# Performance work log

Measured on AMD Instinct MI355X. Metric: run time of the kernel, lower is better.

The kernel has to match this reference:

```python
import jax, jax.numpy as jnp
import numpy as np

NB_CAT = 8192       # nb_category per column
RANK = 16           # low-rank factor dimension
N_COLS = 4          # number of categorical columns (len(embedding_sizes))
N_PAIRS = 1048576   # number of (x, y) index pairs
FRAC_DIAG = 0.9     # fraction_diagonal init


def setup_inputs() -> dict:
    key = jax.random.key(0)
    k1, k2, k3, k4 = jax.random.split(key, 4)
    x = jax.random.randint(k1, (N_PAIRS, N_COLS), 0, NB_CAT, dtype=jnp.int32)
    y = jax.random.randint(k2, (N_PAIRS, N_COLS), 0, NB_CAT, dtype=jnp.int32)
    # params initialized as in the torch module, plus small noise so values are non-degenerate
    std = (FRAC_DIAG * jnp.ones((N_COLS, NB_CAT), dtype=jnp.float32)
           + 0.01 * jax.random.normal(k3, (N_COLS, NB_CAT), dtype=jnp.float32))
    covar_factor = ((1.0 - FRAC_DIAG) / np.float32(np.sqrt(RANK))
                    * jnp.ones((N_COLS, NB_CAT, RANK), dtype=jnp.float32)
                    + 0.01 * jax.random.normal(k4, (N_COLS, NB_CAT, RANK), dtype=jnp.float32))
    return {"x": x, "y": y, "covar_factor": covar_factor, "std": std}


def reference(x, y, covar_factor, std):
    # Build full covariance per column: F @ F.T + diag(std^2)   -> [C, N, N]
    cov = jnp.einsum('cnr,cmr->cnm', covar_factor, covar_factor)
    diag_idx = jnp.arange(cov.shape[1])
    cov = cov.at[:, diag_idx, diag_idx].add(std * std)
    # Gather requested (x, y) entries per column, then reduce (should_reduce=True)
    cols = jnp.arange(cov.shape[0])  # [C]
    vals = cov[cols[None, :], x, y]  # [B, C]
    return vals.sum(axis=-1)         # [B]
```

## Files before the change

### kernel.cpp

```cpp
#include <hip/hip_runtime.h>

#define NB_CAT  8192
#define RANK    16
#define N_COLS  4
#define N_PAIRS 1048576

#define SLICE_ROWS  NB_CAT
#define SLICE_BYTES (SLICE_ROWS * 16)
#define TBL_BYTES   ((size_t)N_COLS * SLICE_BYTES)
#define LDS_BYTES   SLICE_BYTES

typedef float float2v __attribute__((ext_vector_type(2)));

#if defined(__HIP_DEVICE_COMPILE__) && defined(__has_builtin)
#if __has_builtin(__builtin_amdgcn_cvt_pk_f32_fp8) && __has_builtin(__builtin_amdgcn_cvt_pk_fp8_f32)
#define DEV_FP8_HW 1
#endif
#endif

template <int C> __device__ __forceinline__ int comp(const int4& v) {
    if (C == 0) return v.x;
    if (C == 1) return v.y;
    if (C == 2) return v.z;
    return v.w;
}

__device__ __forceinline__ float sw_dec_fp8(unsigned int b) {
    const unsigned int s = b >> 7, e = (b >> 3) & 0xF, m = b & 7;
    float v;
    if (e == 0) v = (float)m * 0.001953125f;
    else        v = ldexpf((float)(8 + m), (int)e - 10);
    return s ? -v : v;
}
__device__ __forceinline__ unsigned int sw_enc_fp8(float f) {
    const unsigned int s = (__float_as_uint(f) >> 31) << 7;
    float a = fabsf(f);
    if (a > 448.f) a = 448.f;
    float q;
    if (a >= 0.015625f) {
        int ex; const float m = frexpf(a, &ex);
        q = ldexpf(rintf(ldexpf(m, 4)), ex - 4);
    } else {
        q = rintf(a * 512.f) * 0.001953125f;
    }
    if (q == 0.f) return s;
    int ex; const float m = frexpf(q, &ex);
    if (ex - 1 < -6) {
        const unsigned int mm = (unsigned int)rintf(q * 512.f);
        return s | (mm & 7);
    }
    const unsigned int e = (unsigned int)(ex - 1 + 7);
    const unsigned int mm = (unsigned int)rintf(ldexpf(m, 4)) & 7;
    return s | (e << 3) | mm;
}

template <bool HI>
__device__ __forceinline__ float2v dec2(unsigned int u) {
#ifdef DEV_FP8_HW
    return __builtin_amdgcn_cvt_pk_f32_fp8((int)u, HI);
#else
    const unsigned int w = HI ? (u >> 16) : u;
    float2v r;
    r.x = sw_dec_fp8(w & 0xFF);
    r.y = sw_dec_fp8((w >> 8) & 0xFF);
    return r;
#endif
}

__device__ __forceinline__ float dot16_fp8(uint4 A, uint4 B, float acc) {
#define TERM(u, v, SEL)                                                        \
    {                                                                          \
        const float2v a = dec2<SEL>((u));                                      \
        const float2v b = dec2<SEL>((v));                                      \
        acc = fmaf(a.x, b.x, acc);                                             \
        acc = fmaf(a.y, b.y, acc);                                             \
    }
    TERM(A.x, B.x, false) TERM(A.x, B.x, true)
    TERM(A.y, B.y, false) TERM(A.y, B.y, true)
    TERM(A.z, B.z, false) TERM(A.z, B.z, true)
    TERM(A.w, B.w, false) TERM(A.w, B.w, true)
#undef TERM
    return acc;
}

__global__ __launch_bounds__(256) void pack_fp8_kernel(
    const float4* __restrict__ src, uint4* __restrict__ dst)
{
    const int r = blockIdx.x * 256 + threadIdx.x;
    const float4 f0 = src[r * 4 + 0];
    const float4 f1 = src[r * 4 + 1];
    const float4 f2 = src[r * 4 + 2];
    const float4 f3 = src[r * 4 + 3];
    uint4 u;
#ifdef DEV_FP8_HW
    int w;
    w = 0;
    w = __builtin_amdgcn_cvt_pk_fp8_f32(f0.x, f0.y, w, false);
    w = __builtin_amdgcn_cvt_pk_fp8_f32(f0.z, f0.w, w, true);
    u.x = (unsigned int)w;
    w = 0;
    w = __builtin_amdgcn_cvt_pk_fp8_f32(f1.x, f1.y, w, false);
    w = __builtin_amdgcn_cvt_pk_fp8_f32(f1.z, f1.w, w, true);
    u.y = (unsigned int)w;
    w = 0;
    w = __builtin_amdgcn_cvt_pk_fp8_f32(f2.x, f2.y, w, false);
    w = __builtin_amdgcn_cvt_pk_fp8_f32(f2.z, f2.w, w, true);
    u.z = (unsigned int)w;
    w = 0;
    w = __builtin_amdgcn_cvt_pk_fp8_f32(f3.x, f3.y, w, false);
    w = __builtin_amdgcn_cvt_pk_fp8_f32(f3.z, f3.w, w, true);
    u.w = (unsigned int)w;
#else
    u.x = sw_enc_fp8(f0.x) | (sw_enc_fp8(f0.y) << 8) | (sw_enc_fp8(f0.z) << 16) | (sw_enc_fp8(f0.w) << 24);
    u.y = sw_enc_fp8(f1.x) | (sw_enc_fp8(f1.y) << 8) | (sw_enc_fp8(f1.z) << 16) | (sw_enc_fp8(f1.w) << 24);
    u.z = sw_enc_fp8(f2.x) | (sw_enc_fp8(f2.y) << 8) | (sw_enc_fp8(f2.z) << 16) | (sw_enc_fp8(f2.w) << 24);
    u.w = sw_enc_fp8(f3.x) | (sw_enc_fp8(f3.y) << 8) | (sw_enc_fp8(f3.z) << 16) | (sw_enc_fp8(f3.w) << 24);
#endif
    dst[r] = u;
}

__global__ __launch_bounds__(1024, 1) void IndexKernel_32238024524411_kernel(
    const int4*  __restrict__ x4,
    const int4*  __restrict__ y4,
    const uint4* __restrict__ tbl,
    const float* __restrict__ stdv,
    float*       __restrict__ out)
{
    extern __shared__ uint4 sh[];

    const int tid  = threadIdx.x;
    const int base = blockIdx.x * 4096 + tid;

    int4 xv[4], yv[4];
#pragma unroll
    for (int j = 0; j < 4; ++j) {
        xv[j] = x4[base + j * 1024];
        yv[j] = y4[base + j * 1024];
    }

    float acc[4] = {0.f, 0.f, 0.f, 0.f};

#pragma unroll
    for (int j = 0; j < 4; ++j) {
        const int4 a = xv[j], b = yv[j];
        if (a.x == b.x) { const float s = stdv[0 * NB_CAT + a.x]; acc[j] = fmaf(s, s, acc[j]); }
        if (a.y == b.y) { const float s = stdv[1 * NB_CAT + a.y]; acc[j] = fmaf(s, s, acc[j]); }
        if (a.z == b.z) { const float s = stdv[2 * NB_CAT + a.z]; acc[j] = fmaf(s, s, acc[j]); }
        if (a.w == b.w) { const float s = stdv[3 * NB_CAT + a.w]; acc[j] = fmaf(s, s, acc[j]); }
    }

#pragma unroll
    for (int it = 0; it < 8; ++it) sh[tid + it * 1024] = tbl[tid + it * 1024];
    asm volatile("s_waitcnt lgkmcnt(0)" ::: "memory");
    __builtin_amdgcn_s_barrier();
    asm volatile("" ::: "memory");

    uint4 t0, t1, t2, t3, t4, t5, t6, t7;

#define PHASE(S)                                                               \
    {                                                                          \
        constexpr int s = (S);                                                 \
        if (s < N_COLS - 1) {                                                  \
            const uint4* nsrc = tbl + (size_t)(s + 1) * SLICE_ROWS;            \
            t0 = nsrc[tid];             t1 = nsrc[tid + 1024];                 \
            t2 = nsrc[tid + 2 * 1024];  t3 = nsrc[tid + 3 * 1024];             \
            t4 = nsrc[tid + 4 * 1024];  t5 = nsrc[tid + 5 * 1024];             \
            t6 = nsrc[tid + 6 * 1024];  t7 = nsrc[tid + 7 * 1024];             \
        }                                                                      \
        asm volatile("" ::: "memory");                                         \
        _Pragma("unroll")                                                      \
        for (int j = 0; j < 4; ++j) {                                          \
            const int a = comp<s>(xv[j]);                                      \
            const int b = comp<s>(yv[j]);                                      \
            acc[j] = dot16_fp8(sh[a], sh[b], acc[j]);                          \
        }                                                                      \
        if (s < N_COLS - 1) {                                                  \
            asm volatile("s_waitcnt lgkmcnt(0)" ::: "memory");                 \
            __builtin_amdgcn_s_barrier();                                      \
            asm volatile("" ::: "memory");                                     \
            sh[tid]            = t0;  sh[tid + 1024]     = t1;                 \
            sh[tid + 2 * 1024] = t2;  sh[tid + 3 * 1024] = t3;                 \
            sh[tid + 4 * 1024] = t4;  sh[tid + 5 * 1024] = t5;                 \
            sh[tid + 6 * 1024] = t6;  sh[tid + 7 * 1024] = t7;                 \
            asm volatile("s_waitcnt lgkmcnt(0)" ::: "memory");                 \
            __builtin_amdgcn_s_barrier();                                      \
            asm volatile("" ::: "memory");                                     \
        }                                                                      \
    }

    PHASE(0) PHASE(1) PHASE(2) PHASE(3)
#undef PHASE

#pragma unroll
    for (int j = 0; j < 4; ++j) {
        out[base + j * 1024] = acc[j];
    }
}

__global__ __launch_bounds__(256) void fallback_kernel(
    const int* __restrict__ x, const int* __restrict__ y,
    const float4* __restrict__ cf, const float* __restrict__ stdv,
    float* __restrict__ out)
{
    const int tid = threadIdx.x;
    const int q = tid & 15, gi = tid >> 4, c = q >> 2, s = q & 3;
    const int p0 = blockIdx.x * 32 + gi, p1 = p0 + 16;
    const int rb = c * NB_CAT;
    const int xi0 = x[p0*4+c], yi0 = y[p0*4+c], xi1 = x[p1*4+c], yi1 = y[p1*4+c];
    const float4 a0 = cf[(size_t)(rb+xi0)*4 + s], b0 = cf[(size_t)(rb+yi0)*4 + s];
    const float4 a1 = cf[(size_t)(rb+xi1)*4 + s], b1 = cf[(size_t)(rb+yi1)*4 + s];
    float v0 = a0.x*b0.x; v0 = fmaf(a0.y,b0.y,v0); v0 = fmaf(a0.z,b0.z,v0); v0 = fmaf(a0.w,b0.w,v0);
    float v1 = a1.x*b1.x; v1 = fmaf(a1.y,b1.y,v1); v1 = fmaf(a1.z,b1.z,v1); v1 = fmaf(a1.w,b1.w,v1);
    if (s == 0 && xi0 == yi0) { float sd = stdv[rb+xi0]; v0 = fmaf(sd,sd,v0); }
    if (s == 0 && xi1 == yi1) { float sd = stdv[rb+yi1]; v1 = fmaf(sd,sd,v1); }
    int t;
    t = __builtin_amdgcn_update_dpp(0, __float_as_int(v0), 0xB1, 0xF, 0xF, true); v0 += __int_as_float(t);
    t = __builtin_amdgcn_update_dpp(0, __float_as_int(v0), 0x4E, 0xF, 0xF, true); v0 += __int_as_float(t);
    t = __builtin_amdgcn_update_dpp(0, __float_as_int(v0), 0x141,0xF, 0xF, true); v0 += __int_as_float(t);
    t = __builtin_amdgcn_update_dpp(0, __float_as_int(v0), 0x128,0xF, 0xF, true); v0 += __int_as_float(t);
    t = __builtin_amdgcn_update_dpp(0, __float_as_int(v1), 0xB1, 0xF, 0xF, true); v1 += __int_as_float(t);
    t = __builtin_amdgcn_update_dpp(0, __float_as_int(v1), 0x4E, 0xF, 0xF, true); v1 += __int_as_float(t);
    t = __builtin_amdgcn_update_dpp(0, __float_as_int(v1), 0x141,0xF, 0xF, true); v1 += __int_as_float(t);
    t = __builtin_amdgcn_update_dpp(0, __float_as_int(v1), 0x128,0xF, 0xF, true); v1 += __int_as_float(t);
    if (q == 0) { out[p0] = v0; out[p1] = v1; }
}

extern "C" void kernel_launch(void* const* d_in, const int* in_sizes, int n_in,
                              void* d_out, int out_size, void* d_ws, size_t ws_size,
                              hipStream_t stream) {
    const int*   x    = (const int*)d_in[0];
    const int*   y    = (const int*)d_in[1];
    const float* cf   = (const float*)d_in[2];
    const float* stdv = (const float*)d_in[3];
    float*       out  = (float*)d_out;

    if (ws_size < TBL_BYTES) {
        fallback_kernel<<<N_PAIRS / 32, 256, 0, stream>>>(
            x, y, (const float4*)cf, stdv, out);
        return;
    }

    (void)hipFuncSetAttribute(
        reinterpret_cast<const void*>(&IndexKernel_32238024524411_kernel),
        hipFuncAttributeMaxDynamicSharedMemorySize, LDS_BYTES);

    pack_fp8_kernel<<<N_COLS * NB_CAT / 256, 256, 0, stream>>>(
        (const float4*)cf, (uint4*)d_ws);

    IndexKernel_32238024524411_kernel<<<N_PAIRS / 4096, 1024, LDS_BYTES, stream>>>(
        (const int4*)x, (const int4*)y, (const uint4*)d_ws, stdv, out);
}
```

Before: 90.13 us.

## Store fp8 factor table planar in LDS and async-load first slice

The pack kernel now writes each column's fp8 factors as four dword planes instead of one 16-byte row per category. The gather kernel therefore reads four 32-bit LDS words per row instead of one 128-bit read, aiming to cut bank conflicts on random row lookups. The first slice is also copied into LDS with global_load_lds before the index loads, so the copy overlaps index fetching. The cost is four times as many LDS read instructions per row, plus reliance on the direct-to-LDS load builtin.

```diff
diff --git a/kernel.cpp b/kernel.cpp
--- a/kernel.cpp
+++ b/kernel.cpp
@@ -15,6 +15,9 @@
 #if defined(__HIP_DEVICE_COMPILE__) && defined(__has_builtin)
 #if __has_builtin(__builtin_amdgcn_cvt_pk_f32_fp8) && __has_builtin(__builtin_amdgcn_cvt_pk_fp8_f32)
 #define DEV_FP8_HW 1
+#endif
+#if __has_builtin(__builtin_amdgcn_global_load_lds)
+#define DEV_GLL 1
 #endif
 #endif
 
@@ -67,7 +70,11 @@
 #endif
 }
 
-__device__ __forceinline__ float dot16_fp8(uint4 A, uint4 B, float acc) {
+__device__ __forceinline__ float dot16_fp8_planar(
+    unsigned int A0, unsigned int A1, unsigned int A2, unsigned int A3,
+    unsigned int B0, unsigned int B1, unsigned int B2, unsigned int B3,
+    float acc)
+{
 #define TERM(u, v, SEL)                                                        \
     {                                                                          \
         const float2v a = dec2<SEL>((u));                                      \
@@ -75,10 +82,10 @@
         acc = fmaf(a.x, b.x, acc);                                             \
         acc = fmaf(a.y, b.y, acc);                                             \
     }
-    TERM(A.x, B.x, false) TERM(A.x, B.x, true)
-    TERM(A.y, B.y, false) TERM(A.y, B.y, true)
-    TERM(A.z, B.z, false) TERM(A.z, B.z, true)
-    TERM(A.w, B.w, false) TERM(A.w, B.w, true)
+    TERM(A0, B0, false) TERM(A0, B0, true)
+    TERM(A1, B1, false) TERM(A1, B1, true)
+    TERM(A2, B2, false) TERM(A2, B2, true)
+    TERM(A3, B3, false) TERM(A3, B3, true)
 #undef TERM
     return acc;
 }
@@ -116,7 +123,14 @@
     u.z = sw_enc_fp8(f2.x) | (sw_enc_fp8(f2.y) << 8) | (sw_enc_fp8(f2.z) << 16) | (sw_enc_fp8(f2.w) << 24);
     u.w = sw_enc_fp8(f3.x) | (sw_enc_fp8(f3.y) << 8) | (sw_enc_fp8(f3.z) << 16) | (sw_enc_fp8(f3.w) << 24);
 #endif
-    dst[r] = u;
+    const int c = r >> 13;
+    const int a = r & (NB_CAT - 1);
+    unsigned int* dw = (unsigned int*)dst;
+    const int base = (c << 15) + a;
+    dw[base]             = u.x;
+    dw[base + 1 * 8192]  = u.y;
+    dw[base + 2 * 8192]  = u.z;
+    dw[base + 3 * 8192]  = u.w;
 }
 
 __global__ __launch_bounds__(1024, 1) void IndexKernel_32238024524411_kernel(
@@ -127,9 +141,23 @@
     float*       __restrict__ out)
 {
     extern __shared__ uint4 sh[];
+    const unsigned int* shw = (const unsigned int*)sh;
 
     const int tid  = threadIdx.x;
     const int base = blockIdx.x * 4096 + tid;
+
+#ifdef DEV_GLL
+#pragma unroll
+    for (int it = 0; it < 8; ++it) {
+        __builtin_amdgcn_global_load_lds(
+            (const __attribute__((address_space(1))) unsigned int*)(tbl + tid + it * 1024),
+            (__attribute__((address_space(3))) unsigned int*)(sh + tid + it * 1024),
+            16, 0, 0);
+    }
+#else
+#pragma unroll
+    for (int it = 0; it < 8; ++it) sh[tid + it * 1024] = tbl[tid + it * 1024];
+#endif
 
     int4 xv[4], yv[4];
 #pragma unroll
@@ -149,9 +177,7 @@
         if (a.w == b.w) { const float s = stdv[3 * NB_CAT + a.w]; acc[j] = fmaf(s, s, acc[j]); }
     }
 
-#pragma unroll
-    for (int it = 0; it < 8; ++it) sh[tid + it * 1024] = tbl[tid + it * 1024];
-    asm volatile("s_waitcnt lgkmcnt(0)" ::: "memory");
+    asm volatile("s_waitcnt vmcnt(0) lgkmcnt(0)" ::: "memory");
     __builtin_amdgcn_s_barrier();
     asm volatile("" ::: "memory");
 
@@ -172,7 +198,15 @@
         for (int j = 0; j < 4; ++j) {                                          \
             const int a = comp<s>(xv[j]);                                      \
             const int b = comp<s>(yv[j]);                                      \
-            acc[j] = dot16_fp8(sh[a], sh[b], acc[j]);                          \
+            const unsigned int A0 = shw[a];                                    \
+            const unsigned int A1 = shw[a + 1 * 8192];                         \
+            const unsigned int A2 = shw[a + 2 * 8192];                         \
+            const unsigned int A3 = shw[a + 3 * 8192];                         \
+            const unsigned int B0 = shw[b];                                    \
+            const unsigned int B1 = shw[b + 1 * 8192];                         \
+            const unsigned int B2 = shw[b + 2 * 8192];                         \
+            const unsigned int B3 = shw[b + 3 * 8192];                         \
+            acc[j] = dot16_fp8_planar(A0, A1, A2, A3, B0, B1, B2, B3, acc[j]); \
         }                                                                      \
         if (s < N_COLS - 1) {                                                  \
             asm volatile("s_waitcnt lgkmcnt(0)" ::: "memory");                 \
```

Result: no change. 89.98 us (-0.2%).

## Split fp8 table into half-rank stages with async global-to-LDS double buffering

Applied to the files above, without the earlier changes.

The pack kernel now stores each column's fp8 factor table as two half-rank planes (8 bytes per row). The main kernel streams eight 64KB stages into a 128KB double-buffered LDS region using global_load_lds where available, gathering 8-element dot products per stage. This replaces the register-staged copy of whole 128KB slices and its extra barriers, letting the next stage's load overlap the current stage's gather. The cost is twice as many gather passes and barriers. It also depends on vmcnt accounting being correct for the direct-to-LDS loads.

```diff
diff --git a/kernel.cpp b/kernel.cpp
--- a/kernel.cpp
+++ b/kernel.cpp
@@ -5,16 +5,18 @@
 #define N_COLS  4
 #define N_PAIRS 1048576
 
-#define SLICE_ROWS  NB_CAT
-#define SLICE_BYTES (SLICE_ROWS * 16)
+#define SLICE_BYTES (NB_CAT * 16)
 #define TBL_BYTES   ((size_t)N_COLS * SLICE_BYTES)
-#define LDS_BYTES   SLICE_BYTES
+#define LDS_BYTES   (128 * 1024)
 
 typedef float float2v __attribute__((ext_vector_type(2)));
 
 #if defined(__HIP_DEVICE_COMPILE__) && defined(__has_builtin)
 #if __has_builtin(__builtin_amdgcn_cvt_pk_f32_fp8) && __has_builtin(__builtin_amdgcn_cvt_pk_fp8_f32)
 #define DEV_FP8_HW 1
+#endif
+#if __has_builtin(__builtin_amdgcn_global_load_lds)
+#define DEV_GLL 1
 #endif
 #endif
 
@@ -67,7 +69,7 @@
 #endif
 }
 
-__device__ __forceinline__ float dot16_fp8(uint4 A, uint4 B, float acc) {
+__device__ __forceinline__ float dot8_fp8(uint2 A, uint2 B, float acc) {
 #define TERM(u, v, SEL)                                                        \
     {                                                                          \
         const float2v a = dec2<SEL>((u));                                      \
@@ -77,8 +79,6 @@
     }
     TERM(A.x, B.x, false) TERM(A.x, B.x, true)
     TERM(A.y, B.y, false) TERM(A.y, B.y, true)
-    TERM(A.z, B.z, false) TERM(A.z, B.z, true)
-    TERM(A.w, B.w, false) TERM(A.w, B.w, true)
 #undef TERM
     return acc;
 }
@@ -116,7 +116,13 @@
     u.z = sw_enc_fp8(f2.x) | (sw_enc_fp8(f2.y) << 8) | (sw_enc_fp8(f2.z) << 16) | (sw_enc_fp8(f2.w) << 24);
     u.w = sw_enc_fp8(f3.x) | (sw_enc_fp8(f3.y) << 8) | (sw_enc_fp8(f3.z) << 16) | (sw_enc_fp8(f3.w) << 24);
 #endif
-    dst[r] = u;
+    const int c = r >> 13;
+    const int a = r & (NB_CAT - 1);
+    uint2* d2 = (uint2*)dst;
+    uint2 w01; w01.x = u.x; w01.y = u.y;
+    uint2 w23; w23.x = u.z; w23.y = u.w;
+    d2[(c << 14) + a]        = w01;
+    d2[(c << 14) + 8192 + a] = w23;
 }
 
 __global__ __launch_bounds__(1024, 1) void IndexKernel_32238024524411_kernel(
@@ -126,10 +132,35 @@
     const float* __restrict__ stdv,
     float*       __restrict__ out)
 {
-    extern __shared__ uint4 sh[];
+    extern __shared__ uint4 sh4[];
 
     const int tid  = threadIdx.x;
     const int base = blockIdx.x * 4096 + tid;
+
+#ifdef DEV_GLL
+#define STAGE(K)                                                               \
+    {                                                                          \
+        const uint4* s_ = tbl + (size_t)(K) * 4096;                            \
+        uint4* d_ = sh4 + (((K) & 1) ? 4096 : 0);                              \
+        _Pragma("unroll")                                                      \
+        for (int it = 0; it < 4; ++it) {                                       \
+            __builtin_amdgcn_global_load_lds(                                  \
+                (const __attribute__((address_space(1))) unsigned int*)(s_ + it * 1024 + tid), \
+                (__attribute__((address_space(3))) unsigned int*)(d_ + it * 1024 + tid),       \
+                16, 0, 0);                                                     \
+        }                                                                      \
+    }
+#else
+#define STAGE(K)                                                               \
+    {                                                                          \
+        const uint4* s_ = tbl + (size_t)(K) * 4096;                            \
+        uint4* d_ = sh4 + (((K) & 1) ? 4096 : 0);                              \
+        _Pragma("unroll")                                                      \
+        for (int it = 0; it < 4; ++it) d_[it * 1024 + tid] = s_[it * 1024 + tid]; \
+    }
+#endif
+
+    STAGE(0) STAGE(1)
 
     int4 xv[4], yv[4];
 #pragma unroll
@@ -149,47 +180,54 @@
         if (a.w == b.w) { const float s = stdv[3 * NB_CAT + a.w]; acc[j] = fmaf(s, s, acc[j]); }
     }
 
-#pragma unroll
-    for (int it = 0; it < 8; ++it) sh[tid + it * 1024] = tbl[tid + it * 1024];
-    asm volatile("s_waitcnt lgkmcnt(0)" ::: "memory");
+    asm volatile("s_waitcnt vmcnt(0) lgkmcnt(0)" ::: "memory");
     __builtin_amdgcn_s_barrier();
     asm volatile("" ::: "memory");
 
-    uint4 t0, t1, t2, t3, t4, t5, t6, t7;
-
-#define PHASE(S)                                                               \
-    {                                                                          \
-        constexpr int s = (S);                                                 \
-        if (s < N_COLS - 1) {                                                  \
-            const uint4* nsrc = tbl + (size_t)(s + 1) * SLICE_ROWS;            \
-            t0 = nsrc[tid];             t1 = nsrc[tid + 1024];                 \
-            t2 = nsrc[tid + 2 * 1024];  t3 = nsrc[tid + 3 * 1024];             \
-            t4 = nsrc[tid + 4 * 1024];  t5 = nsrc[tid + 5 * 1024];             \
-            t6 = nsrc[tid + 6 * 1024];  t7 = nsrc[tid + 7 * 1024];             \
-        }                                                                      \
-        asm volatile("" ::: "memory");                                         \
+#define GATHER(K)                                                              \
+    {                                                                          \
+        constexpr int c_ = (K) >> 1;                                           \
+        const uint2* bp = (const uint2*)(sh4 + (((K) & 1) ? 4096 : 0));        \
         _Pragma("unroll")                                                      \
         for (int j = 0; j < 4; ++j) {                                          \
-            const int a = comp<s>(xv[j]);                                      \
-            const int b = comp<s>(yv[j]);                                      \
-            acc[j] = dot16_fp8(sh[a], sh[b], acc[j]);                          \
+            const int a_ = comp<c_>(xv[j]);                                    \
+            const int b_ = comp<c_>(yv[j]);                                    \
+            const uint2 Av = bp[a_];                                           \
+            const uint2 Bv = bp[b_];                                           \
+            acc[j] = dot8_fp8(Av, Bv, acc[j]);                                 \
         }                                                                      \
-        if (s < N_COLS - 1) {                                                  \
-            asm volatile("s_waitcnt lgkmcnt(0)" ::: "memory");                 \
-            __builtin_amdgcn_s_barrier();                                      \
-            asm volatile("" ::: "memory");                                     \
-            sh[tid]            = t0;  sh[tid + 1024]     = t1;                 \
-            sh[tid + 2 * 1024] = t2;  sh[tid + 3 * 1024] = t3;                 \
-            sh[tid + 4 * 1024] = t4;  sh[tid + 5 * 1024] = t5;                 \
-            sh[tid + 6 * 1024] = t6;  sh[tid + 7 * 1024] = t7;                 \
-            asm volatile("s_waitcnt lgkmcnt(0)" ::: "memory");                 \
-            __builtin_amdgcn_s_barrier();                                      \
-            asm volatile("" ::: "memory");                                     \
-        }                                                                      \
-    }
-
-    PHASE(0) PHASE(1) PHASE(2) PHASE(3)
-#undef PHASE
+    }
+
+#define SYNC_REFILL(KNEXT)                                                     \
+    __builtin_amdgcn_s_barrier();                                              \
+    asm volatile("" ::: "memory");                                             \
+    STAGE(KNEXT)                                                               \
+    asm volatile("s_waitcnt vmcnt(4)" ::: "memory");                           \
+    __builtin_amdgcn_s_barrier();                                              \
+    asm volatile("" ::: "memory");
+
+    GATHER(0)
+    SYNC_REFILL(2)
+    GATHER(1)
+    SYNC_REFILL(3)
+    GATHER(2)
+    SYNC_REFILL(4)
+    GATHER(3)
+    SYNC_REFILL(5)
+    GATHER(4)
+    SYNC_REFILL(6)
+    GATHER(5)
+    SYNC_REFILL(7)
+    GATHER(6)
+    __builtin_amdgcn_s_barrier();
+    asm volatile("s_waitcnt vmcnt(0)" ::: "memory");
+    __builtin_amdgcn_s_barrier();
+    asm volatile("" ::: "memory");
+    GATHER(7)
+
+#undef SYNC_REFILL
+#undef GATHER
+#undef STAGE
 
 #pragma unroll
     for (int j = 0; j < 4; ++j) {
```

Result: no change. 88.56 us (median of 2 runs) (-1.7%).

## Replace LDS-staged table phases with direct global gathers from FP8 table

Applied to the files above, without the earlier changes.

Drops the per-block staging of each 128KB FP8 column slice into LDS, along with its barriers and double-buffered reloads. Each thread now handles one pair and gathers its eight 16-byte rows straight from the 512KB packed table, which should stay resident in L2/MALL. This removes 256 blocks times 512KB of redundant table loads and all the synchronisation. The cost is random, uncoalesced global gathers in place of LDS reads.

```diff
diff --git a/kernel.cpp b/kernel.cpp
--- a/kernel.cpp
+++ b/kernel.cpp
@@ -5,10 +5,8 @@
 #define N_COLS  4
 #define N_PAIRS 1048576
 
-#define SLICE_ROWS  NB_CAT
-#define SLICE_BYTES (SLICE_ROWS * 16)
+#define SLICE_BYTES (NB_CAT * 16)
 #define TBL_BYTES   ((size_t)N_COLS * SLICE_BYTES)
-#define LDS_BYTES   SLICE_BYTES
 
 typedef float float2v __attribute__((ext_vector_type(2)));
 
@@ -17,13 +15,6 @@
 #define DEV_FP8_HW 1
 #endif
 #endif
-
-template <int C> __device__ __forceinline__ int comp(const int4& v) {
-    if (C == 0) return v.x;
-    if (C == 1) return v.y;
-    if (C == 2) return v.z;
-    return v.w;
-}
 
 __device__ __forceinline__ float sw_dec_fp8(unsigned int b) {
     const unsigned int s = b >> 7, e = (b >> 3) & 0xF, m = b & 7;
@@ -119,82 +110,40 @@
     dst[r] = u;
 }
 
-__global__ __launch_bounds__(1024, 1) void IndexKernel_32238024524411_kernel(
+__global__ __launch_bounds__(256, 4) void IndexKernel_32238024524411_kernel(
     const int4*  __restrict__ x4,
     const int4*  __restrict__ y4,
     const uint4* __restrict__ tbl,
     const float* __restrict__ stdv,
     float*       __restrict__ out)
 {
-    extern __shared__ uint4 sh[];
+    const int p = blockIdx.x * 256 + threadIdx.x;
 
-    const int tid  = threadIdx.x;
-    const int base = blockIdx.x * 4096 + tid;
+    const int4 a = x4[p];
+    const int4 b = y4[p];
 
-    int4 xv[4], yv[4];
-#pragma unroll
-    for (int j = 0; j < 4; ++j) {
-        xv[j] = x4[base + j * 1024];
-        yv[j] = y4[base + j * 1024];
-    }
+    const uint4 A0 = tbl[0 * NB_CAT + a.x];
+    const uint4 B0 = tbl[0 * NB_CAT + b.x];
+    const uint4 A1 = tbl[1 * NB_CAT + a.y];
+    const uint4 B1 = tbl[1 * NB_CAT + b.y];
+    const uint4 A2 = tbl[2 * NB_CAT + a.z];
+    const uint4 B2 = tbl[2 * NB_CAT + b.z];
+    const uint4 A3 = tbl[3 * NB_CAT + a.w];
+    const uint4 B3 = tbl[3 * NB_CAT + b.w];
 
-    float acc[4] = {0.f, 0.f, 0.f, 0.f};
+    float acc = 0.f;
 
-#pragma unroll
-    for (int j = 0; j < 4; ++j) {
-        const int4 a = xv[j], b = yv[j];
-        if (a.x == b.x) { const float s = stdv[0 * NB_CAT + a.x]; acc[j] = fmaf(s, s, acc[j]); }
-        if (a.y == b.y) { const float s = stdv[1 * NB_CAT + a.y]; acc[j] = fmaf(s, s, acc[j]); }
-        if (a.z == b.z) { const float s = stdv[2 * NB_CAT + a.z]; acc[j] = fmaf(s, s, acc[j]); }
-        if (a.w == b.w) { const float s = stdv[3 * NB_CAT + a.w]; acc[j] = fmaf(s, s, acc[j]); }
-    }
+    if (a.x == b.x) { const float s = stdv[0 * NB_CAT + a.x]; acc = fmaf(s, s, acc); }
+    if (a.y == b.y) { const float s = stdv[1 * NB_CAT + a.y]; acc = fmaf(s, s, acc); }
+    if (a.z == b.z) { const float s = stdv[2 * NB_CAT + a.z]; acc = fmaf(s, s, acc); }
+    if (a.w == b.w) { const float s = stdv[3 * NB_CAT + a.w]; acc = fmaf(s, s, acc); }
 
-#pragma unroll
-    for (int it = 0; it < 8; ++it) sh[tid + it * 1024] = tbl[tid + it * 1024];
-    asm volatile("s_waitcnt lgkmcnt(0)" ::: "memory");
-    __builtin_amdgcn_s_barrier();
-    asm volatile("" ::: "memory");
+    acc = dot16_fp8(A0, B0, acc);
+    acc = dot16_fp8(A1, B1, acc);
+    acc = dot16_fp8(A2, B2, acc);
+    acc = dot16_fp8(A3, B3, acc);
 
-    uint4 t0, t1, t2, t3, t4, t5, t6, t7;
-
-#define PHASE(S)                                                               \
-    {                                                                          \
-        constexpr int s = (S);                                                 \
-        if (s < N_COLS - 1) {                                                  \
-            const uint4* nsrc = tbl + (size_t)(s + 1) * SLICE_ROWS;            \
-            t0 = nsrc[tid];             t1 = nsrc[tid + 1024];                 \
-            t2 = nsrc[tid + 2 * 1024];  t3 = nsrc[tid + 3 * 1024];             \
-            t4 = nsrc[tid + 4 * 1024];  t5 = nsrc[tid + 5 * 1024];             \
-            t6 = nsrc[tid + 6 * 1024];  t7 = nsrc[tid + 7 * 1024];             \
-        }                                                                      \
-        asm volatile("" ::: "memory");                                         \
-        _Pragma("unroll")                                                      \
-        for (int j = 0; j < 4; ++j) {                                          \
-            const int a = comp<s>(xv[j]);                                      \
-            const int b = comp<s>(yv[j]);                                      \
-            acc[j] = dot16_fp8(sh[a], sh[b], acc[j]);                          \
-        }                                                                      \
-        if (s < N_COLS - 1) {                                                  \
-            asm volatile("s_waitcnt lgkmcnt(0)" ::: "memory");                 \
-            __builtin_amdgcn_s_barrier();                                      \
-            asm volatile("" ::: "memory");                                     \
-            sh[tid]            = t0;  sh[tid + 1024]     = t1;                 \
-            sh[tid + 2 * 1024] = t2;  sh[tid + 3 * 1024] = t3;                 \
-            sh[tid + 4 * 1024] = t4;  sh[tid + 5 * 1024] = t5;                 \
-            sh[tid + 6 * 1024] = t6;  sh[tid + 7 * 1024] = t7;                 \
-            asm volatile("s_waitcnt lgkmcnt(0)" ::: "memory");                 \
-            __builtin_amdgcn_s_barrier();                                      \
-            asm volatile("" ::: "memory");                                     \
-        }                                                                      \
-    }
-
-    PHASE(0) PHASE(1) PHASE(2) PHASE(3)
-#undef PHASE
-
-#pragma unroll
-    for (int j = 0; j < 4; ++j) {
-        out[base + j * 1024] = acc[j];
-    }
+    out[p] = acc;
 }
 
 __global__ __launch_bounds__(256) void fallback_kernel(
@@ -240,13 +189,9 @@
         return;
     }
 
-    (void)hipFuncSetAttribute(
-        reinterpret_cast<const void*>(&IndexKernel_32238024524411_kernel),
-        hipFuncAttributeMaxDynamicSharedMemorySize, LDS_BYTES);
-
     pack_fp8_kernel<<<N_COLS * NB_CAT / 256, 256, 0, stream>>>(
         (const float4*)cf, (uint4*)d_ws);
 
-    IndexKernel_32238024524411_kernel<<<N_PAIRS / 4096, 1024, LDS_BYTES, stream>>>(
+    IndexKernel_32238024524411_kernel<<<N_PAIRS / 256, 256, 0, stream>>>(
         (const int4*)x, (const int4*)y, (const uint4*)d_ws, stdv, out);
 }
```

Result: slower. 109.7 us (+21.7%).
